# Performance work log

Measured on AMD Instinct MI355X. Metric: run time of the kernel, lower is better.

The kernel has to match this reference:

```python
import jax, jax.numpy as jnp
import numpy as np

# ---- module hyperparams derived from init_kwargs (see __init__ math) ----
UP, DOWN = 2, 2              # rint(512/256)
UP_TAPS, DOWN_TAPS = 12, 12  # filter_size(6) * factor(2)
PX0, PX1, PY0, PY1 = 9, 8, 9, 8  # pad_total = 17
SLOPE = 0.01


def _firwin_kaiser(numtaps, cutoff, width, fs):
    # scipy.signal.firwin(numtaps, cutoff, width=width, fs=fs) reimplemented:
    # kaiserord attenuation/beta + windowed sinc, normalized to unit DC gain.
    nyq = 0.5 * fs
    atten = 2.285 * (numtaps - 1) * np.pi * (width / nyq) + 7.95
    if atten > 50:
        beta = 0.1102 * (atten - 8.7)
    elif atten > 21:
        beta = 0.5842 * (atten - 21) ** 0.4 + 0.07886 * (atten - 21)
    else:
        beta = 0.0
    m = np.arange(numtaps) - (numtaps - 1) / 2.0
    c = cutoff / nyq
    h = c * np.sinc(c * m) * np.kaiser(numtaps, beta)
    return (h / h.sum()).astype(np.float32)


def setup_inputs() -> dict:
    key = jax.random.key(0)
    x = jax.random.normal(key, (8, 128, 130, 130), dtype=jnp.float32)
    # design_lowpass_filter(numtaps=12, cutoff=100, width=2*28, fs=512) for both
    up_filter = jnp.asarray(_firwin_kaiser(UP_TAPS, 100.0, 56.0, 512.0))
    down_filter = jnp.asarray(_firwin_kaiser(DOWN_TAPS, 100.0, 56.0, 512.0))
    return {"x": x, "up_filter": up_filter, "down_filter": down_filter}


def reference(x, up_filter, down_filter):
    """filtered_lrelu: FIR 2x upsample -> leaky-relu(0.01) -> FIR 2x downsample.

    Matches upfirdn2d(x, fu, up=2, padding=[9,8,9,8], gain=4) ->
    lrelu(slope=0.01, gain=1.0, clamp=None) -> upfirdn2d(x, fd, down=2).
    """
    B, C, H, W = x.shape
    # Separable 1D filters -> 2D outer product. Upsample gain = up**2.
    fu = jnp.outer(up_filter, up_filter) * float(UP * UP)
    fd = jnp.outer(down_filter, down_filter)
    # flip_filter=False in upfirdn2d means true convolution; lax conv is
    # correlation, so flip the (symmetric) kernels explicitly.
    fu = fu[::-1, ::-1][None, None]  # [1,1,kh,kw]
    fd = fd[::-1, ::-1][None, None]
    xr = x.reshape(B * C, 1, H, W)
    # Zero-stuffing upsample via lhs_dilation gives (H-1)*up+1 samples; the
    # reference zero-stuffs to H*up, so add (up-1) zeros to the hi padding.
    y = jax.lax.conv_general_dilated(
        xr, fu, window_strides=(1, 1),
        padding=((PY0, PY1 + UP - 1), (PX0, PX1 + UP - 1)),
        lhs_dilation=(UP, UP))  # [B*C,1,277,277]
    y = jnp.where(y >= 0, y, y * SLOPE)  # leaky relu, gain=1, no clamp
    # Downsample filter + stride-`down` decimation fused in one conv.
    y = jax.lax.conv_general_dilated(
        y, fd, window_strides=(DOWN, DOWN), padding=((0, 0), (0, 0)))
    return y.reshape(B, C, y.shape[-2], y.shape[-1])  # [8,128,128,128]
```

## Files before the change

kernel.cpp:

```cpp
#include <hip/hip_runtime.h>


#define TOX 32
#define TOY 32
#define XST 44
#define UST 76
#define U_ROWS 42
#define XW_FLOATS (32 * UST)

__global__ __launch_bounds__(256, 7)
void flrelu_fused_kernel(const float* __restrict__ x,
                         const float* __restrict__ upf,
                         const float* __restrict__ downf,
                         float* __restrict__ out) {
    __shared__ __align__(16) float u_s[U_ROWS * UST];
    __shared__ __align__(16) float xw_s[XW_FLOATS];

    const int tid = threadIdx.x;
    const int ch  = blockIdx.z;
    const int ox0 = blockIdx.x * TOX;
    const int oy0 = blockIdx.y * TOY;

    float fu[12], fd[12];
#pragma unroll
    for (int t = 0; t < 12; ++t) fu[t] = upf[t];
#pragma unroll
    for (int t = 0; t < 12; ++t) fd[t] = 2.0f * downf[11 - t];

    {
        const float* __restrict__ xc = x + (size_t)ch * (130 * 130);
        float* xs = xw_s;
        for (int idx = tid; idx < U_ROWS * 22; idx += 256) {
            const int r  = idx / 22;
            const int c2 = idx - r * 22;
            const int gr = oy0 - 4 + r;
            const int gc = ox0 - 4 + 2 * c2;
            float2 v = make_float2(0.f, 0.f);
            if ((unsigned)gr < 130u && (unsigned)gc <= 128u)
                v = *(const float2*)(xc + gr * 130 + gc);
            *(float2*)(xs + r * XST + 2 * c2) = v;
        }
    }
    __syncthreads();

    {
        const float* xs = xw_s;
        const int h0 = tid / 19;
        const int g  = tid - 19 * h0;
        if (tid < 247) {
#pragma unroll
            for (int k = 0; k < 4; ++k) {
                const int h = h0 + 13 * k;
                if (h < U_ROWS) {
                    const float* xr = xs + h * XST + 2 * g;
                    float2 s01 = *(const float2*)(xr);
                    float2 s23 = *(const float2*)(xr + 2);
                    float2 s45 = *(const float2*)(xr + 4);
                    float  s6  = xr[6];
                    float u0 = fu[0]*s45.y + fu[2]*s45.x + fu[4]*s23.y + fu[6]*s23.x + fu[8]*s01.y + fu[10]*s01.x;
                    float u1 = fu[1]*s45.y + fu[3]*s45.x + fu[5]*s23.y + fu[7]*s23.x + fu[9]*s01.y + fu[11]*s01.x;
                    float u2 = fu[0]*s6    + fu[2]*s45.y + fu[4]*s45.x + fu[6]*s23.y + fu[8]*s23.x + fu[10]*s01.y;
                    float u3 = fu[1]*s6    + fu[3]*s45.y + fu[5]*s45.x + fu[7]*s23.y + fu[9]*s23.x + fu[11]*s01.y;
                    *(float4*)(u_s + h * UST + 4 * g) = make_float4(u0, u1, u2, u3);
                }
            }
        }
    }
    __syncthreads();

    if (tid < 152) {
        const int seg = (tid >= UST) ? 1 : 0;
        const int lj  = tid - seg * UST;
        const float* ucol = u_s + (seg * 16) * UST + lj;
        float*       wb   = xw_s + (seg * 16) * UST + lj;
        float r0 = ucol[0*UST], r1 = ucol[1*UST], r2 = ucol[2*UST],
              r3 = ucol[3*UST], r4 = ucol[4*UST];
        float a0 = 0.f, a1 = 0.f, a2 = 0.f, a3 = 0.f, a4 = 0.f, a5 = 0.f;
#pragma unroll
        for (int m = 0; m < 5; ++m) {
            float r5 = ucol[(m + 5) * UST];
            float z0 = fu[0]*r5 + fu[2]*r4 + fu[4]*r3 + fu[6]*r2 + fu[8]*r1 + fu[10]*r0;
            float z1 = fu[1]*r5 + fu[3]*r4 + fu[5]*r3 + fu[7]*r2 + fu[9]*r1 + fu[11]*r0;
            z0 = fmaxf(z0, 0.01f * z0);
            z1 = fmaxf(z1, 0.01f * z1);
            a0 += fd[0]*z0  + fd[1]*z1;
            a1 += fd[2]*z0  + fd[3]*z1;
            a2 += fd[4]*z0  + fd[5]*z1;
            a3 += fd[6]*z0  + fd[7]*z1;
            a4 += fd[8]*z0  + fd[9]*z1;
            a5 += fd[10]*z0 + fd[11]*z1;
            a5 = a4; a4 = a3; a3 = a2; a2 = a1; a1 = a0; a0 = 0.f;
            r0 = r1; r1 = r2; r2 = r3; r3 = r4; r4 = r5;
        }
#pragma unroll
        for (int m = 5; m < 21; ++m) {
            float r5 = ucol[(m + 5) * UST];
            float z0 = fu[0]*r5 + fu[2]*r4 + fu[4]*r3 + fu[6]*r2 + fu[8]*r1 + fu[10]*r0;
            float z1 = fu[1]*r5 + fu[3]*r4 + fu[5]*r3 + fu[7]*r2 + fu[9]*r1 + fu[11]*r0;
            z0 = fmaxf(z0, 0.01f * z0);
            z1 = fmaxf(z1, 0.01f * z1);
            a0 += fd[0]*z0  + fd[1]*z1;
            a1 += fd[2]*z0  + fd[3]*z1;
            a2 += fd[4]*z0  + fd[5]*z1;
            a3 += fd[6]*z0  + fd[7]*z1;
            a4 += fd[8]*z0  + fd[9]*z1;
            a5 += fd[10]*z0 + fd[11]*z1;
            wb[(m - 5) * UST] = a5;
            a5 = a4; a4 = a3; a3 = a2; a2 = a1; a1 = a0; a0 = 0.f;
            r0 = r1; r1 = r2; r2 = r3; r3 = r4; r4 = r5;
        }
    }
    __syncthreads();

    {
        const float* w = xw_s;
        const int oy = tid >> 3;
        const int g  = tid & 7;
        const float* wr = w + oy * UST + 8 * g;
        float4 q0 = *(const float4*)&wr[0];
        float4 q1 = *(const float4*)&wr[4];
        float4 q2 = *(const float4*)&wr[8];
        float4 q3 = *(const float4*)&wr[12];
        float2 e  = *(const float2*)&wr[16];
        float o0v = fd[0]*q0.x + fd[1]*q0.y + fd[2]*q0.z + fd[3]*q0.w
                  + fd[4]*q1.x + fd[5]*q1.y + fd[6]*q1.z + fd[7]*q1.w
                  + fd[8]*q2.x + fd[9]*q2.y + fd[10]*q2.z + fd[11]*q2.w;
        float o1v = fd[0]*q0.z + fd[1]*q0.w + fd[2]*q1.x + fd[3]*q1.y
                  + fd[4]*q1.z + fd[5]*q1.w + fd[6]*q2.x + fd[7]*q2.y
                  + fd[8]*q2.z + fd[9]*q2.w + fd[10]*q3.x + fd[11]*q3.y;
        float o2v = fd[0]*q1.x + fd[1]*q1.y + fd[2]*q1.z + fd[3]*q1.w
                  + fd[4]*q2.x + fd[5]*q2.y + fd[6]*q2.z + fd[7]*q2.w
                  + fd[8]*q3.x + fd[9]*q3.y + fd[10]*q3.z + fd[11]*q3.w;
        float o3v = fd[0]*q1.z + fd[1]*q1.w + fd[2]*q2.x + fd[3]*q2.y
                  + fd[4]*q2.z + fd[5]*q2.w + fd[6]*q3.x + fd[7]*q3.y
                  + fd[8]*q3.z + fd[9]*q3.w + fd[10]*e.x  + fd[11]*e.y;
        float* __restrict__ outc = out + (size_t)ch * (128 * 128);
        *(float4*)(outc + (size_t)(oy0 + oy) * 128 + ox0 + 4 * g) =
            make_float4(o0v, o1v, o2v, o3v);
    }
}

extern "C" void kernel_launch(void* const* d_in, const int* in_sizes, int n_in,
                              void* d_out, int out_size, void* d_ws, size_t ws_size,
                              hipStream_t stream) {
    const float* x     = (const float*)d_in[0];
    const float* upf   = (const float*)d_in[1];
    const float* downf = (const float*)d_in[2];
    float* out = (float*)d_out;

    dim3 grid(128 / TOX, 128 / TOY, 8 * 128);
    dim3 block(256);
    flrelu_fused_kernel<<<grid, block, 0, stream>>>(x, upf, downf, out);
}
```

Before: 169.0 us.

## Double tile height, load input directly into upsample pass, reuse one LDS buffer

Output tile height grows from 32 to 64 rows, which cuts the share of vertical halo rows that must be recomputed per block and halves the block count. The separate LDS staging of the input tile and its barrier are dropped: each thread reads its input samples straight from global memory, using clamped addresses and masks for the borders. The vertical pass now writes its results back into the same LDS buffer at non-overlapping row offsets, so no second buffer is needed. The cost is a longer serial vertical loop run by only 152 threads, and uncoalesced, redundant global reads in the horizontal pass.

```diff
diff --git a/kernel.cpp b/kernel.cpp
--- a/kernel.cpp
+++ b/kernel.cpp
@@ -2,11 +2,9 @@
 
 
 #define TOX 32
-#define TOY 32
-#define XST 44
+#define TOY 64
 #define UST 76
-#define U_ROWS 42
-#define XW_FLOATS (32 * UST)
+#define U_ROWS 74
 
 __global__ __launch_bounds__(256, 7)
 void flrelu_fused_kernel(const float* __restrict__ x,
@@ -14,7 +12,6 @@
                          const float* __restrict__ downf,
                          float* __restrict__ out) {
     __shared__ __align__(16) float u_s[U_ROWS * UST];
-    __shared__ __align__(16) float xw_s[XW_FLOATS];
 
     const int tid = threadIdx.x;
     const int ch  = blockIdx.z;
@@ -29,38 +26,38 @@
 
     {
         const float* __restrict__ xc = x + (size_t)ch * (130 * 130);
-        float* xs = xw_s;
-        for (int idx = tid; idx < U_ROWS * 22; idx += 256) {
-            const int r  = idx / 22;
-            const int c2 = idx - r * 22;
-            const int gr = oy0 - 4 + r;
-            const int gc = ox0 - 4 + 2 * c2;
-            float2 v = make_float2(0.f, 0.f);
-            if ((unsigned)gr < 130u && (unsigned)gc <= 128u)
-                v = *(const float2*)(xc + gr * 130 + gc);
-            *(float2*)(xs + r * XST + 2 * c2) = v;
-        }
-    }
-    __syncthreads();
-
-    {
-        const float* xs = xw_s;
-        const int h0 = tid / 19;
-        const int g  = tid - 19 * h0;
+        const int g   = tid % 19;
+        const int h0  = tid / 19;
+        const int gc0 = ox0 - 4 + 2 * g;
+        const bool c0 = (unsigned)(gc0    ) <= 128u;
+        const bool c2 = (unsigned)(gc0 + 2) <= 128u;
+        const bool c4 = (unsigned)(gc0 + 4) <= 128u;
+        const bool c6 = (unsigned)(gc0 + 6) <= 129u;
+        const int o0 = c0 ? gc0     : 0;
+        const int o2 = c2 ? gc0 + 2 : 0;
+        const int o4 = c4 ? gc0 + 4 : 0;
+        const int o6 = c6 ? gc0 + 6 : 0;
         if (tid < 247) {
 #pragma unroll
-            for (int k = 0; k < 4; ++k) {
+            for (int k = 0; k < 6; ++k) {
                 const int h = h0 + 13 * k;
-                if (h < U_ROWS) {
-                    const float* xr = xs + h * XST + 2 * g;
-                    float2 s01 = *(const float2*)(xr);
-                    float2 s23 = *(const float2*)(xr + 2);
-                    float2 s45 = *(const float2*)(xr + 4);
-                    float  s6  = xr[6];
-                    float u0 = fu[0]*s45.y + fu[2]*s45.x + fu[4]*s23.y + fu[6]*s23.x + fu[8]*s01.y + fu[10]*s01.x;
-                    float u1 = fu[1]*s45.y + fu[3]*s45.x + fu[5]*s23.y + fu[7]*s23.x + fu[9]*s01.y + fu[11]*s01.x;
-                    float u2 = fu[0]*s6    + fu[2]*s45.y + fu[4]*s45.x + fu[6]*s23.y + fu[8]*s23.x + fu[10]*s01.y;
-                    float u3 = fu[1]*s6    + fu[3]*s45.y + fu[5]*s45.x + fu[7]*s23.y + fu[9]*s23.x + fu[11]*s01.y;
+                if (k < 5 || h < U_ROWS) {
+                    const int  gr  = oy0 - 4 + h;
+                    const bool rok = (unsigned)gr < 130u;
+                    const int  rb  = (rok ? gr : 0) * 130;
+                    float2 t01 = *(const float2*)(xc + rb + o0);
+                    float2 t23 = *(const float2*)(xc + rb + o2);
+                    float2 t45 = *(const float2*)(xc + rb + o4);
+                    float  t6  = xc[rb + o6];
+                    const float s0 = c0 ? t01.x : 0.f, s1 = c0 ? t01.y : 0.f;
+                    const float s2 = c2 ? t23.x : 0.f, s3 = c2 ? t23.y : 0.f;
+                    const float s4 = c4 ? t45.x : 0.f, s5 = c4 ? t45.y : 0.f;
+                    const float s6 = c6 ? t6    : 0.f;
+                    float u0 = fu[0]*s5 + fu[2]*s4 + fu[4]*s3 + fu[6]*s2 + fu[8]*s1 + fu[10]*s0;
+                    float u1 = fu[1]*s5 + fu[3]*s4 + fu[5]*s3 + fu[7]*s2 + fu[9]*s1 + fu[11]*s0;
+                    float u2 = fu[0]*s6 + fu[2]*s5 + fu[4]*s4 + fu[6]*s3 + fu[8]*s2 + fu[10]*s1;
+                    float u3 = fu[1]*s6 + fu[3]*s5 + fu[5]*s4 + fu[7]*s3 + fu[9]*s2 + fu[11]*s1;
+                    if (!rok) { u0 = 0.f; u1 = 0.f; u2 = 0.f; u3 = 0.f; }
                     *(float4*)(u_s + h * UST + 4 * g) = make_float4(u0, u1, u2, u3);
                 }
             }
@@ -71,8 +68,8 @@
     if (tid < 152) {
         const int seg = (tid >= UST) ? 1 : 0;
         const int lj  = tid - seg * UST;
-        const float* ucol = u_s + (seg * 16) * UST + lj;
-        float*       wb   = xw_s + (seg * 16) * UST + lj;
+        const float* ucol = u_s + (seg * 32) * UST + lj;
+        float*       wb   = u_s + (seg * 42) * UST + lj;
         float r0 = ucol[0*UST], r1 = ucol[1*UST], r2 = ucol[2*UST],
               r3 = ucol[3*UST], r4 = ucol[4*UST];
         float a0 = 0.f, a1 = 0.f, a2 = 0.f, a3 = 0.f, a4 = 0.f, a5 = 0.f;
@@ -93,7 +90,7 @@
             r0 = r1; r1 = r2; r2 = r3; r3 = r4; r4 = r5;
         }
 #pragma unroll
-        for (int m = 5; m < 21; ++m) {
+        for (int m = 5; m < 37; ++m) {
             float r5 = ucol[(m + 5) * UST];
             float z0 = fu[0]*r5 + fu[2]*r4 + fu[4]*r3 + fu[6]*r2 + fu[8]*r1 + fu[10]*r0;
             float z1 = fu[1]*r5 + fu[3]*r4 + fu[5]*r3 + fu[7]*r2 + fu[9]*r1 + fu[11]*r0;
@@ -113,30 +110,32 @@
     __syncthreads();
 
     {
-        const float* w = xw_s;
-        const int oy = tid >> 3;
-        const int g  = tid & 7;
-        const float* wr = w + oy * UST + 8 * g;
-        float4 q0 = *(const float4*)&wr[0];
-        float4 q1 = *(const float4*)&wr[4];
-        float4 q2 = *(const float4*)&wr[8];
-        float4 q3 = *(const float4*)&wr[12];
-        float2 e  = *(const float2*)&wr[16];
-        float o0v = fd[0]*q0.x + fd[1]*q0.y + fd[2]*q0.z + fd[3]*q0.w
-                  + fd[4]*q1.x + fd[5]*q1.y + fd[6]*q1.z + fd[7]*q1.w
-                  + fd[8]*q2.x + fd[9]*q2.y + fd[10]*q2.z + fd[11]*q2.w;
-        float o1v = fd[0]*q0.z + fd[1]*q0.w + fd[2]*q1.x + fd[3]*q1.y
-                  + fd[4]*q1.z + fd[5]*q1.w + fd[6]*q2.x + fd[7]*q2.y
-                  + fd[8]*q2.z + fd[9]*q2.w + fd[10]*q3.x + fd[11]*q3.y;
-        float o2v = fd[0]*q1.x + fd[1]*q1.y + fd[2]*q1.z + fd[3]*q1.w
-                  + fd[4]*q2.x + fd[5]*q2.y + fd[6]*q2.z + fd[7]*q2.w
-                  + fd[8]*q3.x + fd[9]*q3.y + fd[10]*q3.z + fd[11]*q3.w;
-        float o3v = fd[0]*q1.z + fd[1]*q1.w + fd[2]*q2.x + fd[3]*q2.y
-                  + fd[4]*q2.z + fd[5]*q2.w + fd[6]*q3.x + fd[7]*q3.y
-                  + fd[8]*q3.z + fd[9]*q3.w + fd[10]*e.x  + fd[11]*e.y;
+        const int g = tid & 7;
+        const int t = tid >> 3;
         float* __restrict__ outc = out + (size_t)ch * (128 * 128);
-        *(float4*)(outc + (size_t)(oy0 + oy) * 128 + ox0 + 4 * g) =
-            make_float4(o0v, o1v, o2v, o3v);
+#pragma unroll
+        for (int oyr = 0; oyr < 2; ++oyr) {
+            const float* wr = u_s + (oyr * 42 + t) * UST + 8 * g;
+            float4 q0 = *(const float4*)&wr[0];
+            float4 q1 = *(const float4*)&wr[4];
+            float4 q2 = *(const float4*)&wr[8];
+            float4 q3 = *(const float4*)&wr[12];
+            float2 e  = *(const float2*)&wr[16];
+            float o0v = fd[0]*q0.x + fd[1]*q0.y + fd[2]*q0.z + fd[3]*q0.w
+                      + fd[4]*q1.x + fd[5]*q1.y + fd[6]*q1.z + fd[7]*q1.w
+                      + fd[8]*q2.x + fd[9]*q2.y + fd[10]*q2.z + fd[11]*q2.w;
+            float o1v = fd[0]*q0.z + fd[1]*q0.w + fd[2]*q1.x + fd[3]*q1.y
+                      + fd[4]*q1.z + fd[5]*q1.w + fd[6]*q2.x + fd[7]*q2.y
+                      + fd[8]*q2.z + fd[9]*q2.w + fd[10]*q3.x + fd[11]*q3.y;
+            float o2v = fd[0]*q1.x + fd[1]*q1.y + fd[2]*q1.z + fd[3]*q1.w
+                      + fd[4]*q2.x + fd[5]*q2.y + fd[6]*q2.z + fd[7]*q2.w
+                      + fd[8]*q3.x + fd[9]*q3.y + fd[10]*q3.z + fd[11]*q3.w;
+            float o3v = fd[0]*q1.z + fd[1]*q1.w + fd[2]*q2.x + fd[3]*q2.y
+                      + fd[4]*q2.z + fd[5]*q2.w + fd[6]*q3.x + fd[7]*q3.y
+                      + fd[8]*q3.z + fd[9]*q3.w + fd[10]*e.x  + fd[11]*e.y;
+            *(float4*)(outc + (size_t)(oy0 + oyr * 32 + t) * 128 + ox0 + 4 * g) =
+                make_float4(o0v, o1v, o2v, o3v);
+        }
     }
 }
 
```

Measured after the change: 158.4 us. -6.3%, faster.
